# Performance work log

Hardware: AMD Instinct MI355X
Metric: run time of the kernel (lower is better)

The kernel has to match this reference:

```python
import jax, jax.numpy as jnp
import numpy as np

S, D, H, HD, CQ, CKV, O = 2048, 2048, 16, 128, 96, 512, 2048


def _linear_params(k, fan_in, fan_out):
    kw, kb = jax.random.split(k)
    lim = 1.0 / np.sqrt(fan_in)
    w = jax.random.uniform(kw, (fan_out, fan_in), minval=-lim, maxval=lim, dtype=jnp.float32)
    b = jax.random.uniform(kb, (fan_out,), minval=-lim, maxval=lim, dtype=jnp.float32)
    return w, b


def setup_inputs() -> dict:
    key = jax.random.key(0)
    ks = jax.random.split(key, 8)
    x = jax.random.normal(ks[0], (S, D), dtype=jnp.float32)
    # standard RoPE tables: theta_i = 10000^(-2i/hd), rotate-half layout
    pos = jnp.arange(S, dtype=jnp.float32)[:, None]              # (S, 1)
    inv_freq = 1.0 / (10000.0 ** (jnp.arange(0, HD, 2, dtype=jnp.float32) / HD))  # (HD/2,)
    ang = pos * inv_freq[None, :]                                 # (S, HD/2)
    rope_cos = jnp.concatenate([jnp.cos(ang), jnp.cos(ang)], axis=-1)  # (S, HD)
    rope_sin = jnp.concatenate([jnp.sin(ang), jnp.sin(ang)], axis=-1)  # (S, HD)
    wq_down, bq_down = _linear_params(ks[1], D, CQ)
    wq_up, bq_up = _linear_params(ks[2], CQ, H * HD)
    wkv_down, bkv_down = _linear_params(ks[3], D, CKV)
    wk_up, bk_up = _linear_params(ks[4], CKV, H * HD)
    wv_up, bv_up = _linear_params(ks[5], CKV, H * HD)
    wo, bo = _linear_params(ks[6], H * HD, O)
    return dict(x=x, rope_cos=rope_cos, rope_sin=rope_sin,
                wq_down=wq_down, bq_down=bq_down, wq_up=wq_up, bq_up=bq_up,
                wkv_down=wkv_down, bkv_down=bkv_down, wk_up=wk_up, bk_up=bk_up,
                wv_up=wv_up, bv_up=bv_up, wo=wo, bo=bo)


def _rope(xh, cos, sin):
    # xh: (S, H, hd); cos/sin: (S, hd) broadcast over heads
    half = xh.shape[-1] // 2
    x1, x2 = xh[..., :half], xh[..., half:]
    rot = jnp.concatenate([-x2, x1], axis=-1)
    return xh * cos[:, None, :] + rot * sin[:, None, :]


def reference(x, rope_cos, rope_sin, wq_down, bq_down, wq_up, bq_up,
              wkv_down, bkv_down, wk_up, bk_up, wv_up, bv_up, wo, bo):
    s = x.shape[0]
    # low-rank Q path: down then up (compressed_q_size < head_dim branch)
    c_q = x @ wq_down.T + bq_down                                  # (S, CQ)
    q = (c_q @ wq_up.T + bq_up).reshape(s, H, HD)                  # (S, H, hd)
    q = _rope(q, rope_cos, rope_sin)
    # shared compressed KV path
    c_kv = x @ wkv_down.T + bkv_down                               # (S, CKV)
    k = _rope((c_kv @ wk_up.T + bk_up).reshape(s, H, HD), rope_cos, rope_sin)
    v = (c_kv @ wv_up.T + bv_up).reshape(s, H, HD)
    # scaled dot-product attention per head (softmax in fp32 as in source)
    q = q / jnp.sqrt(jnp.asarray(HD, q.dtype))
    logits = jnp.einsum('shd,Shd->hsS', q, k)                      # (H, S, S)
    weights = jax.nn.softmax(logits.astype(jnp.float32), axis=-1).astype(logits.dtype)
    attn = jnp.einsum('hsS,Shd->shd', weights, v).reshape(s, H * HD)
    return attn @ wo.T + bo                                        # (S, O)
```

## Files before the change

### kernel.cpp

```cpp
#include <hip/hip_runtime.h>
#include <cstdint>
#include <cstddef>

typedef unsigned short u16;
typedef float f32x4 __attribute__((ext_vector_type(4)));
typedef short s16x8 __attribute__((ext_vector_type(8)));

#define DI __device__ __forceinline__

static constexpr int S_  = 2048;
static constexpr int D_  = 2048;
static constexpr int H_  = 16;
static constexpr int HD_ = 128;
static constexpr int HHD = 2048;
static constexpr int CQP = 128;
static constexpr int NCAT = 640;
static constexpr int CKV_ = 512;

DI u16 f2bf(float f) {
  unsigned u = __float_as_uint(f);
  u += 0x7fffu + ((u >> 16) & 1u);
  return (u16)(u >> 16);
}
DI float bf2f(u16 h) { return __uint_as_float(((unsigned)h) << 16); }

DI void store_c(float* C, long long i, float v) { C[i] = v; }
DI void store_c(u16* C, long long i, float v) { C[i] = f2bf(v); }

template <int CTRL>
DI float dppf(float x) {
  return __uint_as_float((unsigned)__builtin_amdgcn_mov_dpp(
      (int)__float_as_uint(x), CTRL, 0xf, 0xf, true));
}
DI float red_max16(float x) {
  x = fmaxf(x, dppf<0xB1>(x));
  x = fmaxf(x, dppf<0x4E>(x));
  x = fmaxf(x, dppf<0x141>(x));
  x = fmaxf(x, dppf<0x140>(x));
  return x;
}
DI float red_sum16(float x) {
  x += dppf<0xB1>(x);
  x += dppf<0x4E>(x);
  x += dppf<0x141>(x);
  x += dppf<0x140>(x);
  return x;
}

#define GLD16(g, l)                                                        \
  __builtin_amdgcn_global_load_lds(                                        \
      (__attribute__((address_space(1))) void*)(void*)(const void*)(g),    \
      (__attribute__((address_space(3))) void*)(l), 16, 0, 0)

template <typename OutT, int BCOL, int BROW, int BN>
__global__ __launch_bounds__(256) void gemm_bt(
    const u16* __restrict__ A, const u16* __restrict__ B, OutT* __restrict__ C,
    const float* __restrict__ bias_col, const float* __restrict__ bias_row,
    int K, int lda, int ldb, int ldc,
    long long sA, long long sB, long long sC) {
  constexpr int MI = (BN == 128) ? 4 : 2;
  constexpr int NI = 4;
  constexpr int NCH = 8 + BN / 16;
  constexpr int NC4 = NCH / 4;
  __shared__ __align__(16) u16 As[2 * 128 * 32];
  __shared__ __align__(16) u16 Bs[2 * BN * 32];
  const int tid  = threadIdx.x;
  const int w    = tid >> 6;
  const int lane = tid & 63;
  const int lr   = lane & 15;
  const int lq   = lane >> 4;
  const long long m0 = (long long)blockIdx.y * 128;
  const long long n0 = (long long)blockIdx.x * BN;
  A += (long long)blockIdx.z * sA;
  B += (long long)blockIdx.z * sB;
  C += (long long)blockIdx.z * sC;
  const int wr = (BN == 128) ? (w >> 1) * 64 : w * 32;
  const int wc = (BN == 128) ? (w & 1) * 64 : 0;

  f32x4 acc[MI][NI];
#pragma unroll
  for (int i = 0; i < MI; ++i)
#pragma unroll
    for (int j = 0; j < NI; ++j)
#pragma unroll
      for (int r = 0; r < 4; ++r) acc[i][j][r] = 0.f;

  const int rch = lane >> 2, cch = (lane & 3) * 8;
  const u16* gsrc[NC4];
  u16* ldst[NC4];
  int bstep[NC4];
#pragma unroll
  for (int ci = 0; ci < NC4; ++ci) {
    const int c = w + ci * 4;
    if (c < 8) {
      gsrc[ci] = A + (m0 + c * 16 + rch) * lda + cch;
      ldst[ci] = &As[c * 512];
      bstep[ci] = 128 * 32;
    } else {
      gsrc[ci] = B + (n0 + (c - 8) * 16 + rch) * ldb + cch;
      ldst[ci] = &Bs[(c - 8) * 512];
      bstep[ci] = BN * 32;
    }
  }
  auto stage = [&](int kt, int b) {
#pragma unroll
    for (int ci = 0; ci < NC4; ++ci) GLD16(gsrc[ci] + kt, ldst[ci] + b * bstep[ci]);
  };

  stage(0, 0);
  int cur = 0;
  for (int kt = 0; kt < K; kt += 32) {
    __syncthreads();
    if (kt + 32 < K) stage(kt + 32, cur ^ 1);
    const u16* Ab = &As[cur * 128 * 32];
    const u16* Bb = &Bs[cur * BN * 32];

    s16x8 af[MI], bfr[NI];
#pragma unroll
    for (int tm = 0; tm < MI; ++tm)
      af[tm] = *(const s16x8*)&Ab[(wr + tm * 16 + lr) * 32 + lq * 8];
#pragma unroll
    for (int tn = 0; tn < NI; ++tn)
      bfr[tn] = *(const s16x8*)&Bb[(wc + tn * 16 + lr) * 32 + lq * 8];
#pragma unroll
    for (int tm = 0; tm < MI; ++tm)
#pragma unroll
      for (int tn = 0; tn < NI; ++tn)
        acc[tm][tn] = __builtin_amdgcn_mfma_f32_16x16x32_bf16(af[tm], bfr[tn],
                                                              acc[tm][tn], 0, 0, 0);
    cur ^= 1;
  }

#pragma unroll
  for (int tm = 0; tm < MI; ++tm)
#pragma unroll
    for (int tn = 0; tn < NI; ++tn) {
      const long long col = n0 + wc + tn * 16 + lr;
      float bc = BCOL ? bias_col[col] : 0.f;
#pragma unroll
      for (int r = 0; r < 4; ++r) {
        const long long row = m0 + wr + tm * 16 + lq * 4 + r;
        float v = acc[tm][tn][r] + bc;
        if (BROW) v += bias_row[row];
        store_c(C, row * (long long)ldc + col, v);
      }
    }
}

DI void store4(float* d, long long e, float4 s) { *(float4*)(d + e) = s; }
DI void store4(u16* d, long long e, float4 s) {
  unsigned lo = (unsigned)f2bf(s.x) | ((unsigned)f2bf(s.y) << 16);
  unsigned hi = (unsigned)f2bf(s.z) | ((unsigned)f2bf(s.w) << 16);
  *(uint2*)(d + e) = make_uint2(lo, hi);
}
template <typename OutT>
__global__ __launch_bounds__(256) void combine_z(
    const float* __restrict__ p, long long zs, int nz,
    const float* __restrict__ bias, OutT* __restrict__ dst, int ldc, int n4) {
  int i = blockIdx.x * 256 + threadIdx.x;
  if (i >= n4) return;
  long long e = (long long)i * 4;
  float4 s = *(const float4*)(p + e);
  for (int z = 1; z < nz; ++z) {
    float4 t = *(const float4*)(p + (long long)z * zs + e);
    s.x += t.x; s.y += t.y; s.z += t.z; s.w += t.w;
  }
  int c = (int)(e % ldc);
  s.x += bias[c]; s.y += bias[c + 1]; s.z += bias[c + 2]; s.w += bias[c + 3];
  store4(dst, e, s);
}

__global__ __launch_bounds__(512, 2) void flash_attn(
    const u16* __restrict__ Q, const u16* __restrict__ Kg,
    const u16* __restrict__ Vt, u16* __restrict__ Og) {
  __shared__ __align__(16) u16 Ks[128 * 128];
  __shared__ __align__(16) u16 Vs[128 * 128];
  __shared__ __align__(16) u16 Ps[128 * 132];
  const int h = blockIdx.x;
  const int t = blockIdx.y;
  const int tid = threadIdx.x;
  const int w = tid >> 6, lane = tid & 63, lr = lane & 15, lq = lane >> 4;
  const int qg = t * 128 + w * 16;
  const int rsub = w * 4 + (lane >> 4);
  const int csw  = (lane & 15) ^ (rsub & 7);

  s16x8 qf[4];
#pragma unroll
  for (int kst = 0; kst < 4; ++kst)
    qf[kst] = *(const s16x8*)&Q[(size_t)(qg + lr) * HHD + h * HD_ + kst * 32 + lq * 8];

  f32x4 oacc[8];
  float m[4], l[4];
#pragma unroll
  for (int r = 0; r < 4; ++r) { m[r] = -3.0e38f; l[r] = 0.f; }
#pragma unroll
  for (int f = 0; f < 8; ++f)
#pragma unroll
    for (int r = 0; r < 4; ++r) oacc[f][r] = 0.f;

  auto stage_k = [&](int j) {
#pragma unroll
    for (int i = 0; i < 4; ++i) {
      const u16* s0 = Kg + (size_t)(j * 128 + i * 32 + rsub) * HHD + h * HD_ + csw * 8;
      GLD16(s0, &Ks[(i * 32 + w * 4) * 128]);
    }
  };
  auto stage_v = [&](int j) {
#pragma unroll
    for (int i = 0; i < 4; ++i) {
      const u16* s0 = Vt + (size_t)(h * HD_ + i * 32 + rsub) * S_ + j * 128 + csw * 8;
      GLD16(s0, &Vs[(i * 32 + w * 4) * 128]);
    }
  };

  stage_k(0);
  stage_v(0);
  __syncthreads();

  for (int j = 0; j < 16; ++j) {
    f32x4 sacc[8];
#pragma unroll
    for (int f = 0; f < 8; ++f)
#pragma unroll
      for (int r = 0; r < 4; ++r) sacc[f][r] = 0.f;
#pragma unroll
    for (int kst = 0; kst < 4; ++kst)
#pragma unroll
      for (int f = 0; f < 8; ++f) {
        s16x8 kf = *(const s16x8*)
            &Ks[(f * 16 + lr) * 128 + (((kst * 4 + lq) ^ (lr & 7)) << 3)];
        sacc[f] = __builtin_amdgcn_mfma_f32_16x16x32_bf16(qf[kst], kf, sacc[f], 0, 0, 0);
      }

#pragma unroll
    for (int r = 0; r < 4; ++r) {
      float mx = sacc[0][r];
#pragma unroll
      for (int f = 1; f < 8; ++f) mx = fmaxf(mx, sacc[f][r]);
      mx = red_max16(mx);
      float mn = fmaxf(m[r], mx);
      float al = __expf(m[r] - mn);
      m[r] = mn;
      float sum = 0.f;
#pragma unroll
      for (int f = 0; f < 8; ++f) {
        float p = __expf(sacc[f][r] - mn);
        sacc[f][r] = p;
        sum += p;
      }
      sum = red_sum16(sum);
      l[r] = l[r] * al + sum;
#pragma unroll
      for (int f = 0; f < 8; ++f) oacc[f][r] *= al;
    }

#pragma unroll
    for (int f = 0; f < 8; ++f)
#pragma unroll
      for (int r = 0; r < 4; ++r)
        Ps[(w * 16 + lq * 4 + r) * 132 + f * 16 + lr] = f2bf(sacc[f][r]);

    __syncthreads();
    if (j < 15) stage_k(j + 1);

#pragma unroll
    for (int kst = 0; kst < 4; ++kst) {
      s16x8 pa = *(const s16x8*)&Ps[(w * 16 + lr) * 132 + kst * 32 + lq * 8];
#pragma unroll
      for (int f = 0; f < 8; ++f) {
        s16x8 vf = *(const s16x8*)
            &Vs[(f * 16 + lr) * 128 + (((kst * 4 + lq) ^ (lr & 7)) << 3)];
        oacc[f] = __builtin_amdgcn_mfma_f32_16x16x32_bf16(pa, vf, oacc[f], 0, 0, 0);
      }
    }
    __syncthreads();
    if (j < 15) stage_v(j + 1);
  }

  float inv[4];
#pragma unroll
  for (int r = 0; r < 4; ++r) inv[r] = 1.f / l[r];
#pragma unroll
  for (int f = 0; f < 8; ++f)
#pragma unroll
    for (int r = 0; r < 4; ++r)
      Og[(size_t)(qg + lq * 4 + r) * HHD + h * HD_ + f * 16 + lr] =
          f2bf(oacc[f][r] * inv[r]);
}

DI void cast4(const float* __restrict__ s, u16* __restrict__ d, int v) {
  float4 f = ((const float4*)s)[v];
  unsigned lo = (unsigned)f2bf(f.x) | ((unsigned)f2bf(f.y) << 16);
  unsigned hi = (unsigned)f2bf(f.z) | ((unsigned)f2bf(f.w) << 16);
  ((uint2*)d)[v] = make_uint2(lo, hi);
}
DI void store_bf4(u16* __restrict__ d, int i, float4 f) {
  unsigned lo = (unsigned)f2bf(f.x) | ((unsigned)f2bf(f.y) << 16);
  unsigned hi = (unsigned)f2bf(f.z) | ((unsigned)f2bf(f.w) << 16);
  *(uint2*)(d + i) = make_uint2(lo, hi);
}
static constexpr int PV_XB   = 1048576;
static constexpr int PV_WCAT = 327680;
static constexpr int PV_WQU  = 65536;
static constexpr int PV_WKU  = 262144;
static constexpr int PV_WVU  = 262144;
static constexpr int PV_WOB  = 1048576;
static constexpr int PV_BCAT = 160;
static constexpr int PV_TOT  = PV_XB + PV_WCAT + PV_WQU + PV_WKU + PV_WVU + PV_WOB + PV_BCAT;

__global__ __launch_bounds__(256) void prep(
    const float* __restrict__ x, const float* __restrict__ wqd_s,
    const float* __restrict__ wkvd_s, const float* __restrict__ wqu_s,
    const float* __restrict__ wku_s, const float* __restrict__ wvu_s,
    const float* __restrict__ wo_s, const float* __restrict__ bqd_s,
    const float* __restrict__ bkvd_s,
    u16* __restrict__ xb, u16* __restrict__ wcat, u16* __restrict__ wqu,
    u16* __restrict__ wku, u16* __restrict__ wvu, u16* __restrict__ wob,
    float* __restrict__ bcat) {
  int v = blockIdx.x * 256 + threadIdx.x;
  if (v >= PV_TOT) return;
  if (v < PV_XB) { cast4(x, xb, v); return; }
  v -= PV_XB;
  if (v < PV_WCAT) {
    int i = v * 4, n = i >> 11, k = i & 2047;
    float4 o = make_float4(0.f, 0.f, 0.f, 0.f);
    if (n < 96)       o = *(const float4*)&wqd_s[n * D_ + k];
    else if (n >= 128) o = *(const float4*)&wkvd_s[(n - 128) * D_ + k];
    store_bf4(wcat, i, o);
    return;
  }
  v -= PV_WCAT;
  if (v < PV_WQU) {
    int i = v * 4, r = i >> 7, c = i & 127;
    float4 o = (c < 96) ? *(const float4*)&wqu_s[r * 96 + c]
                        : make_float4(0.f, 0.f, 0.f, 0.f);
    store_bf4(wqu, i, o);
    return;
  }
  v -= PV_WQU;
  if (v < PV_WKU) { cast4(wku_s, wku, v); return; }
  v -= PV_WKU;
  if (v < PV_WVU) { cast4(wvu_s, wvu, v); return; }
  v -= PV_WVU;
  if (v < PV_WOB) { cast4(wo_s, wob, v); return; }
  v -= PV_WOB;
  {
    int i = v * 4;
    float4 o;
    float* po = &o.x;
#pragma unroll
    for (int jj = 0; jj < 4; ++jj) {
      int e = i + jj;
      po[jj] = (e < 96) ? bqd_s[e] : (e < 128 ? 0.f : bkvd_s[e - 128]);
    }
    *(float4*)&bcat[i] = o;
  }
}

__global__ __launch_bounds__(256) void rope2(u16* __restrict__ qb,
                                             u16* __restrict__ kb,
                                             const float* __restrict__ cs,
                                             const float* __restrict__ sn) {
  int id = blockIdx.x * 256 + threadIdx.x;
  const bool isq = id < S_ * H_ * 64;
  if (!isq) id -= S_ * H_ * 64;
  u16* X = isq ? qb : kb;
  const float scale = isq ? 0.08838834764831845f : 1.0f;
  int d = id & 63;
  int h = (id >> 6) & 15;
  int s = id >> 10;
  long long b = (long long)s * HHD + h * HD_ + d;
  float x1 = bf2f(X[b]), x2 = bf2f(X[b + 64]);
  int cb = s * HD_ + d;
  float o1 = (x1 * cs[cb] - x2 * sn[cb]) * scale;
  float o2 = (x2 * cs[cb + 64] + x1 * sn[cb + 64]) * scale;
  X[b] = f2bf(o1);
  X[b + 64] = f2bf(o2);
}

extern "C" void kernel_launch(void* const* d_in, const int* in_sizes, int n_in,
                              void* d_out, int out_size, void* d_ws, size_t ws_size,
                              hipStream_t stream) {
  (void)in_sizes; (void)n_in; (void)out_size; (void)ws_size;
  const float* x        = (const float*)d_in[0];
  const float* rc       = (const float*)d_in[1];
  const float* rs       = (const float*)d_in[2];
  const float* wq_down  = (const float*)d_in[3];
  const float* bq_down  = (const float*)d_in[4];
  const float* wq_up    = (const float*)d_in[5];
  const float* bq_up    = (const float*)d_in[6];
  const float* wkv_down = (const float*)d_in[7];
  const float* bkv_down = (const float*)d_in[8];
  const float* wk_up    = (const float*)d_in[9];
  const float* bk_up    = (const float*)d_in[10];
  const float* wv_up    = (const float*)d_in[11];
  const float* bv_up    = (const float*)d_in[12];
  const float* wo       = (const float*)d_in[13];
  const float* bo       = (const float*)d_in[14];
  float* out = (float*)d_out;

  char* ws = (char*)d_ws;
  size_t off = 0;
  auto alloc = [&](size_t bytes) -> void* {
    off = (off + 255) & ~(size_t)255;
    void* p = ws + off;
    off += bytes;
    return p;
  };

  u16* xb      = (u16*)alloc((size_t)S_ * D_ * 2);
  u16* wcat    = (u16*)alloc((size_t)NCAT * D_ * 2);
  float* bcat  = (float*)alloc(NCAT * 4);
  u16* wqu     = (u16*)alloc((size_t)HHD * CQP * 2);
  u16* wku     = (u16*)alloc((size_t)HHD * CKV_ * 2);
  u16* wvu     = (u16*)alloc((size_t)HHD * CKV_ * 2);
  u16* wob     = (u16*)alloc((size_t)D_ * HHD * 2);
  u16* ccat    = (u16*)alloc((size_t)S_ * NCAT * 2);
  float* pcat  = (float*)alloc((size_t)4 * S_ * NCAT * 4);
  u16* qb      = (u16*)alloc((size_t)S_ * HHD * 2);
  u16* kb      = (u16*)alloc((size_t)S_ * HHD * 2);
  u16* vT      = (u16*)alloc((size_t)HHD * S_ * 2);
  u16* attnb   = (u16*)alloc((size_t)S_ * HHD * 2);

  prep<<<(PV_TOT + 255) / 256, 256, 0, stream>>>(
      x, wq_down, wkv_down, wq_up, wk_up, wv_up, wo, bq_down, bkv_down,
      xb, wcat, wqu, wku, wvu, wob, bcat);

  gemm_bt<float, 0, 0, 64><<<dim3(NCAT / 64, 16, 4), 256, 0, stream>>>(
      xb, wcat, pcat, nullptr, nullptr, 512, D_, D_, NCAT,
      512, 512, (long long)S_ * NCAT);
  combine_z<u16><<<(S_ * NCAT / 4 + 255) / 256, 256, 0, stream>>>(
      pcat, (long long)S_ * NCAT, 4, bcat, ccat, NCAT, S_ * NCAT / 4);

  gemm_bt<u16, 1, 0, 128><<<dim3(16, 16, 1), 256, 0, stream>>>(
      ccat, wqu, qb, bq_up, nullptr, CQP, NCAT, CQP, HHD, 0, 0, 0);
  gemm_bt<u16, 1, 0, 128><<<dim3(16, 16, 1), 256, 0, stream>>>(
      ccat + CQP, wku, kb, bk_up, nullptr, CKV_, NCAT, CKV_, HHD, 0, 0, 0);
  gemm_bt<u16, 0, 1, 128><<<dim3(16, 16, 1), 256, 0, stream>>>(
      wvu, ccat + CQP, vT, nullptr, bv_up, CKV_, CKV_, NCAT, S_, 0, 0, 0);

  rope2<<<(2 * S_ * H_ * 64) / 256, 256, 0, stream>>>(qb, kb, rc, rs);

  flash_attn<<<dim3(H_, S_ / 128, 1), 512, 0, stream>>>(qb, kb, vT, attnb);

  gemm_bt<float, 1, 0, 128><<<dim3(16, 16, 1), 256, 0, stream>>>(
      attnb, wob, out, bo, nullptr, HHD, HHD, HHD, D_, 0, 0, 0);
}
```

Baseline: 286.7 us.

## Split attention over KV halves, fuse up-projections, split-K output GEMM

The three up-projection GEMMs become one launch (up3) dispatched by blockIdx.z. Flash attention is restructured to 256 threads with each wave handling 32 query rows. The KV range is split into two halves written as fp32 partials with m/l, merged by a new combine kernel, and the P tile reuses the K shared buffer instead of a separate Ps array. Softmax switches to exp2 with the log2e factor folded into the Q scale, and the output projection uses split-K=2 plus a reduction kernel. This adds parallelism for small grids at the cost of extra launches and fp32 partial traffic.

After: 329.9 us. +15.1%, slower.

```diff
diff --git a/kernel.cpp b/kernel.cpp
--- a/kernel.cpp
+++ b/kernel.cpp
@@ -16,6 +16,7 @@
 static constexpr int CQP = 128;
 static constexpr int NCAT = 640;
 static constexpr int CKV_ = 512;
+static constexpr float QSCALE = 0.12751743360294163f;
 
 DI u16 f2bf(float f) {
   unsigned u = __float_as_uint(f);
@@ -53,17 +54,16 @@
       (__attribute__((address_space(3))) void*)(l), 16, 0, 0)
 
 template <typename OutT, int BCOL, int BROW, int BN>
-__global__ __launch_bounds__(256) void gemm_bt(
-    const u16* __restrict__ A, const u16* __restrict__ B, OutT* __restrict__ C,
-    const float* __restrict__ bias_col, const float* __restrict__ bias_row,
-    int K, int lda, int ldb, int ldc,
-    long long sA, long long sB, long long sC) {
+DI void gemm_core(u16* __restrict__ Asm, u16* __restrict__ Bsm,
+                  const u16* __restrict__ A, const u16* __restrict__ B,
+                  OutT* __restrict__ C,
+                  const float* __restrict__ bias_col,
+                  const float* __restrict__ bias_row,
+                  int K, int lda, int ldb, int ldc) {
   constexpr int MI = (BN == 128) ? 4 : 2;
   constexpr int NI = 4;
   constexpr int NCH = 8 + BN / 16;
   constexpr int NC4 = NCH / 4;
-  __shared__ __align__(16) u16 As[2 * 128 * 32];
-  __shared__ __align__(16) u16 Bs[2 * BN * 32];
   const int tid  = threadIdx.x;
   const int w    = tid >> 6;
   const int lane = tid & 63;
@@ -71,9 +71,6 @@
   const int lq   = lane >> 4;
   const long long m0 = (long long)blockIdx.y * 128;
   const long long n0 = (long long)blockIdx.x * BN;
-  A += (long long)blockIdx.z * sA;
-  B += (long long)blockIdx.z * sB;
-  C += (long long)blockIdx.z * sC;
   const int wr = (BN == 128) ? (w >> 1) * 64 : w * 32;
   const int wc = (BN == 128) ? (w & 1) * 64 : 0;
 
@@ -94,11 +91,11 @@
     const int c = w + ci * 4;
     if (c < 8) {
       gsrc[ci] = A + (m0 + c * 16 + rch) * lda + cch;
-      ldst[ci] = &As[c * 512];
+      ldst[ci] = &Asm[c * 512];
       bstep[ci] = 128 * 32;
     } else {
       gsrc[ci] = B + (n0 + (c - 8) * 16 + rch) * ldb + cch;
-      ldst[ci] = &Bs[(c - 8) * 512];
+      ldst[ci] = &Bsm[(c - 8) * 512];
       bstep[ci] = BN * 32;
     }
   }
@@ -112,8 +109,8 @@
   for (int kt = 0; kt < K; kt += 32) {
     __syncthreads();
     if (kt + 32 < K) stage(kt + 32, cur ^ 1);
-    const u16* Ab = &As[cur * 128 * 32];
-    const u16* Bb = &Bs[cur * BN * 32];
+    const u16* Ab = &Asm[cur * 128 * 32];
+    const u16* Bb = &Bsm[cur * BN * 32];
 
     s16x8 af[MI], bfr[NI];
 #pragma unroll
@@ -145,6 +142,38 @@
         store_c(C, row * (long long)ldc + col, v);
       }
     }
+}
+
+template <typename OutT, int BCOL, int BROW, int BN>
+__global__ __launch_bounds__(256) void gemm_bt(
+    const u16* __restrict__ A, const u16* __restrict__ B, OutT* __restrict__ C,
+    const float* __restrict__ bias_col, const float* __restrict__ bias_row,
+    int K, int lda, int ldb, int ldc,
+    long long sA, long long sB, long long sC) {
+  __shared__ __align__(16) u16 As[2 * 128 * 32];
+  __shared__ __align__(16) u16 Bs[2 * BN * 32];
+  gemm_core<OutT, BCOL, BROW, BN>(
+      As, Bs, A + (long long)blockIdx.z * sA, B + (long long)blockIdx.z * sB,
+      C + (long long)blockIdx.z * sC, bias_col, bias_row, K, lda, ldb, ldc);
+}
+
+__global__ __launch_bounds__(256, 3) void up3(
+    const u16* __restrict__ ccat, const u16* __restrict__ wqu,
+    const u16* __restrict__ wku, const u16* __restrict__ wvu,
+    const float* __restrict__ bq_up, const float* __restrict__ bk_up,
+    const float* __restrict__ bv_up,
+    u16* __restrict__ qb, u16* __restrict__ kb, u16* __restrict__ vT) {
+  __shared__ __align__(16) u16 As[2 * 128 * 32];
+  __shared__ __align__(16) u16 Bs[2 * 128 * 32];
+  if (blockIdx.z == 0)
+    gemm_core<u16, 1, 0, 128>(As, Bs, ccat, wqu, qb, bq_up, nullptr,
+                              CQP, NCAT, CQP, HHD);
+  else if (blockIdx.z == 1)
+    gemm_core<u16, 1, 0, 128>(As, Bs, ccat + CQP, wku, kb, bk_up, nullptr,
+                              CKV_, NCAT, CKV_, HHD);
+  else
+    gemm_core<u16, 0, 1, 128>(As, Bs, wvu, ccat + CQP, vT, nullptr, bv_up,
+                              CKV_, CKV_, NCAT, S_);
 }
 
 DI void store4(float* d, long long e, float4 s) { *(float4*)(d + e) = s; }
@@ -170,122 +199,184 @@
   store4(dst, e, s);
 }
 
-__global__ __launch_bounds__(512, 2) void flash_attn(
+__global__ __launch_bounds__(256, 2) void flash_attn(
     const u16* __restrict__ Q, const u16* __restrict__ Kg,
-    const u16* __restrict__ Vt, u16* __restrict__ Og) {
+    const u16* __restrict__ Vt, float* __restrict__ Op, float* __restrict__ ml) {
   __shared__ __align__(16) u16 Ks[128 * 128];
   __shared__ __align__(16) u16 Vs[128 * 128];
-  __shared__ __align__(16) u16 Ps[128 * 132];
   const int h = blockIdx.x;
   const int t = blockIdx.y;
+  const int kspl = blockIdx.z;
   const int tid = threadIdx.x;
   const int w = tid >> 6, lane = tid & 63, lr = lane & 15, lq = lane >> 4;
-  const int qg = t * 128 + w * 16;
-  const int rsub = w * 4 + (lane >> 4);
-  const int csw  = (lane & 15) ^ (rsub & 7);
-
-  s16x8 qf[4];
-#pragma unroll
-  for (int kst = 0; kst < 4; ++kst)
-    qf[kst] = *(const s16x8*)&Q[(size_t)(qg + lr) * HHD + h * HD_ + kst * 32 + lq * 8];
-
-  f32x4 oacc[8];
-  float m[4], l[4];
-#pragma unroll
-  for (int r = 0; r < 4; ++r) { m[r] = -3.0e38f; l[r] = 0.f; }
-#pragma unroll
-  for (int f = 0; f < 8; ++f)
-#pragma unroll
-    for (int r = 0; r < 4; ++r) oacc[f][r] = 0.f;
+  const int qg = t * 128 + w * 32;
+  const int tr = tid >> 4;
+  const int csw = (tid & 15) ^ (tr & 7);
+
+  s16x8 qf[2][4];
+#pragma unroll
+  for (int mi = 0; mi < 2; ++mi)
+#pragma unroll
+    for (int kst = 0; kst < 4; ++kst)
+      qf[mi][kst] = *(const s16x8*)&Q[(size_t)(qg + mi * 16 + lr) * HHD +
+                                      h * HD_ + kst * 32 + lq * 8];
+
+  f32x4 oacc[2][8];
+  float m[2][4], l[2][4];
+#pragma unroll
+  for (int mi = 0; mi < 2; ++mi) {
+#pragma unroll
+    for (int r = 0; r < 4; ++r) { m[mi][r] = -1.0e38f; l[mi][r] = 0.f; }
+#pragma unroll
+    for (int f = 0; f < 8; ++f)
+#pragma unroll
+      for (int r = 0; r < 4; ++r) oacc[mi][f][r] = 0.f;
+  }
 
   auto stage_k = [&](int j) {
-#pragma unroll
-    for (int i = 0; i < 4; ++i) {
-      const u16* s0 = Kg + (size_t)(j * 128 + i * 32 + rsub) * HHD + h * HD_ + csw * 8;
-      GLD16(s0, &Ks[(i * 32 + w * 4) * 128]);
-    }
+    const u16* s0 = Kg + (size_t)(j * 128 + tr) * HHD + h * HD_ + csw * 8;
+#pragma unroll
+    for (int i = 0; i < 8; ++i)
+      GLD16(s0 + (size_t)i * 16 * HHD, &Ks[i * 2048 + w * 512]);
   };
   auto stage_v = [&](int j) {
-#pragma unroll
-    for (int i = 0; i < 4; ++i) {
-      const u16* s0 = Vt + (size_t)(h * HD_ + i * 32 + rsub) * S_ + j * 128 + csw * 8;
-      GLD16(s0, &Vs[(i * 32 + w * 4) * 128]);
-    }
+    const u16* s0 = Vt + (size_t)(h * HD_ + tr) * S_ + j * 128 + csw * 8;
+#pragma unroll
+    for (int i = 0; i < 8; ++i)
+      GLD16(s0 + (size_t)i * 16 * S_, &Vs[i * 2048 + w * 512]);
   };
 
-  stage_k(0);
-  stage_v(0);
-  __syncthreads();
-
-  for (int j = 0; j < 16; ++j) {
-    f32x4 sacc[8];
-#pragma unroll
-    for (int f = 0; f < 8; ++f)
-#pragma unroll
-      for (int r = 0; r < 4; ++r) sacc[f][r] = 0.f;
+  const int j0 = kspl * 8;
+  stage_k(j0);
+  stage_v(j0);
+
+  for (int jj = 0; jj < 8; ++jj) {
+    __syncthreads();
+
+    f32x4 sacc[2][8];
+#pragma unroll
+    for (int mi = 0; mi < 2; ++mi)
+#pragma unroll
+      for (int f = 0; f < 8; ++f)
+#pragma unroll
+        for (int r = 0; r < 4; ++r) sacc[mi][f][r] = 0.f;
 #pragma unroll
     for (int kst = 0; kst < 4; ++kst)
 #pragma unroll
       for (int f = 0; f < 8; ++f) {
         s16x8 kf = *(const s16x8*)
             &Ks[(f * 16 + lr) * 128 + (((kst * 4 + lq) ^ (lr & 7)) << 3)];
-        sacc[f] = __builtin_amdgcn_mfma_f32_16x16x32_bf16(qf[kst], kf, sacc[f], 0, 0, 0);
+        sacc[0][f] = __builtin_amdgcn_mfma_f32_16x16x32_bf16(qf[0][kst], kf,
+                                                             sacc[0][f], 0, 0, 0);
+        sacc[1][f] = __builtin_amdgcn_mfma_f32_16x16x32_bf16(qf[1][kst], kf,
+                                                             sacc[1][f], 0, 0, 0);
       }
 
 #pragma unroll
-    for (int r = 0; r < 4; ++r) {
-      float mx = sacc[0][r];
-#pragma unroll
-      for (int f = 1; f < 8; ++f) mx = fmaxf(mx, sacc[f][r]);
-      mx = red_max16(mx);
-      float mn = fmaxf(m[r], mx);
-      float al = __expf(m[r] - mn);
-      m[r] = mn;
-      float sum = 0.f;
-#pragma unroll
-      for (int f = 0; f < 8; ++f) {
-        float p = __expf(sacc[f][r] - mn);
-        sacc[f][r] = p;
-        sum += p;
+    for (int mi = 0; mi < 2; ++mi)
+#pragma unroll
+      for (int r = 0; r < 4; ++r) {
+        float mx = sacc[mi][0][r];
+#pragma unroll
+        for (int f = 1; f < 8; ++f) mx = fmaxf(mx, sacc[mi][f][r]);
+        mx = red_max16(mx);
+        float mn = fmaxf(m[mi][r], mx);
+        float al = exp2f(m[mi][r] - mn);
+        m[mi][r] = mn;
+        float sum = 0.f;
+#pragma unroll
+        for (int f = 0; f < 8; ++f) {
+          float p = exp2f(sacc[mi][f][r] - mn);
+          sacc[mi][f][r] = p;
+          sum += p;
+        }
+        sum = red_sum16(sum);
+        l[mi][r] = l[mi][r] * al + sum;
+#pragma unroll
+        for (int f = 0; f < 8; ++f) oacc[mi][f][r] *= al;
       }
-      sum = red_sum16(sum);
-      l[r] = l[r] * al + sum;
-#pragma unroll
-      for (int f = 0; f < 8; ++f) oacc[f][r] *= al;
-    }
-
-#pragma unroll
-    for (int f = 0; f < 8; ++f)
-#pragma unroll
-      for (int r = 0; r < 4; ++r)
-        Ps[(w * 16 + lq * 4 + r) * 132 + f * 16 + lr] = f2bf(sacc[f][r]);
 
     __syncthreads();
-    if (j < 15) stage_k(j + 1);
+
+#pragma unroll
+    for (int mi = 0; mi < 2; ++mi)
+#pragma unroll
+      for (int r = 0; r < 4; ++r) {
+        const int q = w * 32 + mi * 16 + lq * 4 + r;
+#pragma unroll
+        for (int f = 0; f < 8; ++f) {
+          const int ch = (2 * f + (lr >> 3)) ^ (q & 7);
+          Ks[q * 128 + ch * 8 + (lr & 7)] = f2bf(sacc[mi][f][r]);
+        }
+      }
+
+    __syncthreads();
 
 #pragma unroll
     for (int kst = 0; kst < 4; ++kst) {
-      s16x8 pa = *(const s16x8*)&Ps[(w * 16 + lr) * 132 + kst * 32 + lq * 8];
+      s16x8 pa0 = *(const s16x8*)
+          &Ks[(w * 32 + lr) * 128 + (((kst * 4 + lq) ^ (lr & 7)) << 3)];
+      s16x8 pa1 = *(const s16x8*)
+          &Ks[(w * 32 + 16 + lr) * 128 + (((kst * 4 + lq) ^ (lr & 7)) << 3)];
 #pragma unroll
       for (int f = 0; f < 8; ++f) {
         s16x8 vf = *(const s16x8*)
             &Vs[(f * 16 + lr) * 128 + (((kst * 4 + lq) ^ (lr & 7)) << 3)];
-        oacc[f] = __builtin_amdgcn_mfma_f32_16x16x32_bf16(pa, vf, oacc[f], 0, 0, 0);
+        oacc[0][f] = __builtin_amdgcn_mfma_f32_16x16x32_bf16(pa0, vf,
+                                                             oacc[0][f], 0, 0, 0);
+        oacc[1][f] = __builtin_amdgcn_mfma_f32_16x16x32_bf16(pa1, vf,
+                                                             oacc[1][f], 0, 0, 0);
       }
     }
+
     __syncthreads();
-    if (j < 15) stage_v(j + 1);
-  }
-
-  float inv[4];
-#pragma unroll
-  for (int r = 0; r < 4; ++r) inv[r] = 1.f / l[r];
-#pragma unroll
-  for (int f = 0; f < 8; ++f)
-#pragma unroll
-    for (int r = 0; r < 4; ++r)
-      Og[(size_t)(qg + lq * 4 + r) * HHD + h * HD_ + f * 16 + lr] =
-          f2bf(oacc[f][r] * inv[r]);
+    if (jj < 7) {
+      stage_k(j0 + jj + 1);
+      stage_v(j0 + jj + 1);
+    }
+  }
+
+#pragma unroll
+  for (int mi = 0; mi < 2; ++mi) {
+#pragma unroll
+    for (int r = 0; r < 4; ++r) {
+      const int row = qg + mi * 16 + lq * 4 + r;
+      if (lr == 0) {
+        float* p = &ml[((size_t)(kspl * S_ + row) * H_ + h) * 2];
+        p[0] = m[mi][r];
+        p[1] = l[mi][r];
+      }
+#pragma unroll
+      for (int f = 0; f < 8; ++f)
+        Op[(size_t)(kspl * S_ + row) * HHD + h * HD_ + f * 16 + lr] =
+            oacc[mi][f][r];
+    }
+  }
+}
+
+__global__ __launch_bounds__(256) void flash_combine(
+    const float* __restrict__ Op, const float* __restrict__ ml,
+    u16* __restrict__ attnb) {
+  int i = blockIdx.x * 256 + threadIdx.x;
+  long long e = (long long)i * 4;
+  int s = (int)(e >> 11);
+  int h = ((int)e & 2047) >> 7;
+  const float* p0 = &ml[((size_t)s * H_ + h) * 2];
+  const float* p1 = &ml[((size_t)(S_ + s) * H_ + h) * 2];
+  float m0 = p0[0], l0 = p0[1], m1 = p1[0], l1 = p1[1];
+  float M = fmaxf(m0, m1);
+  float w0 = exp2f(m0 - M), w1 = exp2f(m1 - M);
+  float inv = 1.f / (w0 * l0 + w1 * l1);
+  float4 a = *(const float4*)&Op[e];
+  float4 b = *(const float4*)&Op[(size_t)S_ * HHD + e];
+  float4 o;
+  o.x = (w0 * a.x + w1 * b.x) * inv;
+  o.y = (w0 * a.y + w1 * b.y) * inv;
+  o.z = (w0 * a.z + w1 * b.z) * inv;
+  o.w = (w0 * a.w + w1 * b.w) * inv;
+  unsigned lo = (unsigned)f2bf(o.x) | ((unsigned)f2bf(o.y) << 16);
+  unsigned hi = (unsigned)f2bf(o.z) | ((unsigned)f2bf(o.w) << 16);
+  *(uint2*)(attnb + e) = make_uint2(lo, hi);
 }
 
 DI void cast4(const float* __restrict__ s, u16* __restrict__ d, int v) {
@@ -294,7 +385,7 @@
   unsigned hi = (unsigned)f2bf(f.z) | ((unsigned)f2bf(f.w) << 16);
   ((uint2*)d)[v] = make_uint2(lo, hi);
 }
-DI void store_bf4(u16* __restrict__ d, int i, float4 f) {
+DI void store_bf4(u16* __restrict__ d, long long i, float4 f) {
   unsigned lo = (unsigned)f2bf(f.x) | ((unsigned)f2bf(f.y) << 16);
   unsigned hi = (unsigned)f2bf(f.z) | ((unsigned)f2bf(f.w) << 16);
   *(uint2*)(d + i) = make_uint2(lo, hi);
@@ -324,7 +415,7 @@
   if (v < PV_WCAT) {
     int i = v * 4, n = i >> 11, k = i & 2047;
     float4 o = make_float4(0.f, 0.f, 0.f, 0.f);
-    if (n < 96)       o = *(const float4*)&wqd_s[n * D_ + k];
+    if (n < 96)        o = *(const float4*)&wqd_s[n * D_ + k];
     else if (n >= 128) o = *(const float4*)&wkvd_s[(n - 128) * D_ + k];
     store_bf4(wcat, i, o);
     return;
@@ -365,7 +456,7 @@
   const bool isq = id < S_ * H_ * 64;
   if (!isq) id -= S_ * H_ * 64;
   u16* X = isq ? qb : kb;
-  const float scale = isq ? 0.08838834764831845f : 1.0f;
+  const float scale = isq ? QSCALE : 1.0f;
   int d = id & 63;
   int h = (id >> 6) & 15;
   int s = id >> 10;
@@ -416,11 +507,15 @@
   u16* wvu     = (u16*)alloc((size_t)HHD * CKV_ * 2);
   u16* wob     = (u16*)alloc((size_t)D_ * HHD * 2);
   u16* ccat    = (u16*)alloc((size_t)S_ * NCAT * 2);
-  float* pcat  = (float*)alloc((size_t)4 * S_ * NCAT * 4);
   u16* qb      = (u16*)alloc((size_t)S_ * HHD * 2);
   u16* kb      = (u16*)alloc((size_t)S_ * HHD * 2);
   u16* vT      = (u16*)alloc((size_t)HHD * S_ * 2);
   u16* attnb   = (u16*)alloc((size_t)S_ * HHD * 2);
+  float* Op    = (float*)alloc((size_t)2 * S_ * HHD * 4);
+  float* ml    = (float*)alloc((size_t)2 * S_ * H_ * 2 * 4);
+  float* pool  = (float*)alloc((size_t)2 * S_ * D_ * 4);
+  float* pcat  = pool;
+  float* pout  = pool;
 
   prep<<<(PV_TOT + 255) / 256, 256, 0, stream>>>(
       x, wq_down, wkv_down, wq_up, wk_up, wv_up, wo, bq_down, bkv_down,
@@ -432,17 +527,17 @@
   combine_z<u16><<<(S_ * NCAT / 4 + 255) / 256, 256, 0, stream>>>(
       pcat, (long long)S_ * NCAT, 4, bcat, ccat, NCAT, S_ * NCAT / 4);
 
-  gemm_bt<u16, 1, 0, 128><<<dim3(16, 16, 1), 256, 0, stream>>>(
-      ccat, wqu, qb, bq_up, nullptr, CQP, NCAT, CQP, HHD, 0, 0, 0);
-  gemm_bt<u16, 1, 0, 128><<<dim3(16, 16, 1), 256, 0, stream>>>(
-      ccat + CQP, wku, kb, bk_up, nullptr, CKV_, NCAT, CKV_, HHD, 0, 0, 0);
-  gemm_bt<u16, 0, 1, 128><<<dim3(16, 16, 1), 256, 0, stream>>>(
-      wvu, ccat + CQP, vT, nullptr, bv_up, CKV_, CKV_, NCAT, S_, 0, 0, 0);
+  up3<<<dim3(16, 16, 3), 256, 0, stream>>>(
+      ccat, wqu, wku, wvu, bq_up, bk_up, bv_up, qb, kb, vT);
 
   rope2<<<(2 * S_ * H_ * 64) / 256, 256, 0, stream>>>(qb, kb, rc, rs);
 
-  flash_attn<<<dim3(H_, S_ / 128, 1), 512, 0, stream>>>(qb, kb, vT, attnb);
-
-  gemm_bt<float, 1, 0, 128><<<dim3(16, 16, 1), 256, 0, stream>>>(
-      attnb, wob, out, bo, nullptr, HHD, HHD, HHD, D_, 0, 0, 0);
-}
+  flash_attn<<<dim3(H_, S_ / 128, 2), 256, 0, stream>>>(qb, kb, vT, Op, ml);
+  flash_combine<<<(S_ * HHD / 4) / 256, 256, 0, stream>>>(Op, ml, attnb);
+
+  gemm_bt<float, 0, 0, 128><<<dim3(16, 16, 2), 256, 0, stream>>>(
+      attnb, wob, pout, nullptr, nullptr, 1024, HHD, HHD, D_,
+      1024, 1024, (long long)S_ * D_);
+  combine_z<float><<<(S_ * D_ / 4 + 255) / 256, 256, 0, stream>>>(
+      pout, (long long)S_ * D_, 2, bo, out, D_, S_ * D_ / 4);
+}
```
